# Kernel optimization log

Hardware: AMD Instinct MI355X
Metric: run time of the kernel (lower is better)

Reference implementation:

```python
import math
import jax, jax.numpy as jnp
import numpy as np

N_EMBD = 1024
N_HEAD = 16
HEAD_DIM = N_EMBD // N_HEAD
B, T = 4, 2048
LN_EPS = 1e-5


def setup_inputs() -> dict:
    key = jax.random.key(0)
    ks = jax.random.split(key, 20)
    s = 0.02
    d = {
        'x': jax.random.normal(ks[0], (B, T, N_EMBD), jnp.float32),
        'Wq': jax.random.normal(ks[1], (N_EMBD, N_EMBD), jnp.float32) * s,
        'bq': jnp.zeros((N_EMBD,), jnp.float32),
        'Wk': jax.random.normal(ks[2], (N_EMBD, N_EMBD), jnp.float32) * s,
        'bk': jnp.zeros((N_EMBD,), jnp.float32),
        'Wv': jax.random.normal(ks[3], (N_EMBD, N_EMBD), jnp.float32) * s,
        'bv': jnp.zeros((N_EMBD,), jnp.float32),
        'Wo': jax.random.normal(ks[4], (N_EMBD, N_EMBD), jnp.float32) * s,
        'bo': jnp.zeros((N_EMBD,), jnp.float32),
        'ln1_g': jnp.ones((N_EMBD,), jnp.float32),
        'ln1_b': jnp.zeros((N_EMBD,), jnp.float32),
        'ln2_g': jnp.ones((N_EMBD,), jnp.float32),
        'ln2_b': jnp.zeros((N_EMBD,), jnp.float32),
        'W_fc': jax.random.normal(ks[5], (N_EMBD, 4 * N_EMBD), jnp.float32) * s,
        'b_fc': jnp.zeros((4 * N_EMBD,), jnp.float32),
        'W_proj': jax.random.normal(ks[6], (4 * N_EMBD, N_EMBD), jnp.float32) * s,
        'b_proj': jnp.zeros((N_EMBD,), jnp.float32),
    }
    return d


def _layernorm(x, g, b):
    mu = jnp.mean(x, axis=-1, keepdims=True)
    var = jnp.var(x, axis=-1, keepdims=True)
    return (x - mu) * jax.lax.rsqrt(var + LN_EPS) * g + b


def _new_gelu(x):
    c = math.sqrt(2.0 / math.pi)
    return 0.5 * x * (1.0 + jnp.tanh(c * (x + 0.044715 * x ** 3)))


def _attn(x, Wq, bq, Wk, bk, Wv, bv, Wo, bo):
    Bq, Tq, C = x.shape
    def heads(y):  # (B,T,C) -> (B,H,T,D)
        return y.reshape(Bq, Tq, N_HEAD, HEAD_DIM).transpose(0, 2, 1, 3)
    q = heads(x @ Wq + bq)
    k = heads(x @ Wk + bk)
    v = heads(x @ Wv + bv)
    scores = jnp.einsum('bhqd,bhkd->bhqk', q, k) / math.sqrt(HEAD_DIM)
    causal = jnp.tril(jnp.ones((Tq, Tq), bool))
    scores = jnp.where(causal, scores, -jnp.inf)
    w = jax.nn.softmax(scores, axis=-1)
    av = jnp.einsum('bhqk,bhkd->bhqd', w, v)
    av = av.transpose(0, 2, 1, 3).reshape(Bq, Tq, C)
    return av @ Wo + bo


def reference(x, Wq, bq, Wk, bk, Wv, bv, Wo, bo, ln1_g, ln1_b, ln2_g, ln2_b, W_fc, b_fc, W_proj, b_proj):
    x = x + _attn(_layernorm(x, ln1_g, ln1_b), Wq, bq, Wk, bk, Wv, bv, Wo, bo)
    h = _layernorm(x, ln2_g, ln2_b)
    x = x + (_new_gelu(h @ W_fc + b_fc) @ W_proj + b_proj)
    return x
```

## Files before the change

### kernel.cpp

```cpp
#include <hip/hip_runtime.h>

typedef __attribute__((ext_vector_type(8))) short short8;
typedef __attribute__((ext_vector_type(4))) short short4v;
typedef __attribute__((ext_vector_type(4))) float floatx4;
typedef unsigned short u16;

#define MFMA16(a,b,c) __builtin_amdgcn_mfma_f32_16x16x32_bf16(a,b,c,0,0,0)

typedef const __attribute__((address_space(1))) void* gas1;
typedef __attribute__((address_space(3))) void* las3;
static __device__ __forceinline__ void glds16(const void* g, void* l){
  __builtin_amdgcn_global_load_lds((gas1)g, (las3)l, 16, 0, 0);
}

static __device__ __forceinline__ u16 f2b(float f){
  union { float f; unsigned int u; } c; c.f = f;
  unsigned int u = c.u;
  u += 0x7fffu + ((u >> 16) & 1u);
  return (u16)(u >> 16);
}

__global__ __launch_bounds__(256) void transpose_cvt(
    const float* __restrict__ W, u16* __restrict__ Wt, int K, int N){
  __shared__ float tile[32][33];
  const int tx = threadIdx.x & 31;
  const int ty = threadIdx.x >> 5;
  const int nx = blockIdx.x * 32, kx = blockIdx.y * 32;
  #pragma unroll
  for (int i = ty; i < 32; i += 8)
    tile[i][tx] = W[(size_t)(kx + i) * N + nx + tx];
  __syncthreads();
  #pragma unroll
  for (int i = ty; i < 32; i += 8)
    Wt[(size_t)(nx + i) * K + kx + tx] = f2b(tile[tx][i]);
}

__global__ __launch_bounds__(256) void ln_kernel(
    const float* __restrict__ x, const float* __restrict__ g,
    const float* __restrict__ b, u16* __restrict__ out){
  const int row = blockIdx.x, tid = threadIdx.x;
  const float4 v = reinterpret_cast<const float4*>(x + (size_t)row * 1024)[tid];
  float s  = v.x + v.y + v.z + v.w;
  float s2 = v.x*v.x + v.y*v.y + v.z*v.z + v.w*v.w;
  #pragma unroll
  for (int off = 1; off < 64; off <<= 1){
    s  += __shfl_xor(s,  off);
    s2 += __shfl_xor(s2, off);
  }
  __shared__ float red[8];
  const int wave = tid >> 6, lane = tid & 63;
  if (lane == 0){ red[wave] = s; red[4 + wave] = s2; }
  __syncthreads();
  s  = red[0] + red[1] + red[2] + red[3];
  s2 = red[4] + red[5] + red[6] + red[7];
  const float mu  = s * (1.f/1024.f);
  const float var = s2 * (1.f/1024.f) - mu * mu;
  const float rs  = rsqrtf(var + 1e-5f);
  const float4 gg = reinterpret_cast<const float4*>(g)[tid];
  const float4 bb = reinterpret_cast<const float4*>(b)[tid];
  ushort4 o;
  o.x = f2b((v.x - mu) * rs * gg.x + bb.x);
  o.y = f2b((v.y - mu) * rs * gg.y + bb.y);
  o.z = f2b((v.z - mu) * rs * gg.z + bb.z);
  o.w = f2b((v.w - mu) * rs * gg.w + bb.w);
  reinterpret_cast<ushort4*>(out + (size_t)row * 1024)[tid] = o;
}

__global__ __launch_bounds__(256) void bias_concat(
    const float* __restrict__ bq, const float* __restrict__ bk,
    const float* __restrict__ bv, float* __restrict__ o){
  const int i = blockIdx.x * 256 + threadIdx.x;
  if (i < 1024) o[i] = bq[i];
  else if (i < 2048) o[i] = bk[i - 1024];
  else if (i < 3072) o[i] = bv[i - 2048];
}

template<bool GELU, bool RES, bool OUTBF, bool QKVMODE>
__global__ __launch_bounds__(256) void gemm128(
    const u16* __restrict__ A, const u16* __restrict__ Bt,
    const float* __restrict__ bias, const float* __restrict__ bias2,
    const float* __restrict__ bias3,
    const float* __restrict__ res,
    float* __restrict__ outF, u16* __restrict__ outB,
    u16* __restrict__ vtb,
    int M, int N, int K)
{
  __shared__ __attribute__((aligned(16))) u16 sA[2][128 * 32];
  __shared__ __attribute__((aligned(16))) u16 sB[2][128 * 32];
  const int tid  = threadIdx.x;
  const int wave = tid >> 6, lane = tid & 63, quad = lane >> 4, l16 = lane & 15;
  const int m0 = blockIdx.x * 128, n0 = blockIdx.y * 128;
  const int wm = (wave >> 1) * 64, wn = (wave & 1) * 64;

  const int scol = ((lane & 3) ^ ((lane >> 3) & 3)) * 8;
  const size_t aoff = (size_t)(m0 + wave*32 + (lane >> 2)) * K + scol;
  const size_t boff = (size_t)(n0 + wave*32 + (lane >> 2)) * K + scol;
  const size_t half = (size_t)16 * K;
  u16* alp = sA[0] + wave * 1024;
  u16* blp = sB[0] + wave * 1024;
  const int qx = (quad ^ ((l16 >> 1) & 3)) * 8;

  floatx4 acc[4][4];
  #pragma unroll
  for (int i = 0; i < 4; i++)
    #pragma unroll
    for (int nt = 0; nt < 4; nt++) acc[i][nt] = floatx4{0.f,0.f,0.f,0.f};

  for (int k0 = 0; k0 < K; k0 += 64){
    #pragma unroll
    for (int c = 0; c < 2; c++){
      glds16(A  + aoff + k0 + c*32,        alp + c*4096);
      glds16(A  + aoff + k0 + c*32 + half, alp + c*4096 + 512);
      glds16(Bt + boff + k0 + c*32,        blp + c*4096);
      glds16(Bt + boff + k0 + c*32 + half, blp + c*4096 + 512);
    }
    __syncthreads();
    #pragma unroll
    for (int c = 0; c < 2; c++){
      short8 af[4], bf[4];
      #pragma unroll
      for (int i = 0; i < 4; i++)
        af[i] = *reinterpret_cast<const short8*>(&sA[c][(wm + i*16 + l16)*32 + qx]);
      #pragma unroll
      for (int nt = 0; nt < 4; nt++)
        bf[nt] = *reinterpret_cast<const short8*>(&sB[c][(wn + nt*16 + l16)*32 + qx]);
      #pragma unroll
      for (int i = 0; i < 4; i++)
        #pragma unroll
        for (int nt = 0; nt < 4; nt++)
          acc[i][nt] = MFMA16(af[i], bf[nt], acc[i][nt]);
    }
    __syncthreads();
  }

  if (QKVMODE && n0 >= 2048){
    #pragma unroll
    for (int nt = 0; nt < 4; nt++){
      const int hd = n0 + wn + nt*16 + l16 - 2048;
      const float bi = bias3[hd];
      u16* vcol = vtb + (size_t)(hd >> 6) * 131072 + (size_t)(hd & 63) * 2048;
      #pragma unroll
      for (int i = 0; i < 4; i++){
        const int t0 = m0 + wm + i*16 + quad*4;
        const int bb = t0 >> 11, tt = t0 & 2047;
        short4v pk;
        #pragma unroll
        for (int r = 0; r < 4; r++) pk[r] = (short)f2b(acc[i][nt][r] + bi);
        *reinterpret_cast<short4v*>(vcol + (size_t)bb * 2097152 + tt) = pk;
      }
    }
    return;
  }

  #pragma unroll
  for (int nt = 0; nt < 4; nt++){
    const int col = n0 + wn + nt*16 + l16;
    float bi;
    if (QKVMODE) bi = (col < 1024) ? bias[col] : bias2[col-1024];
    else         bi = bias[col];
    #pragma unroll
    for (int i = 0; i < 4; i++){
      #pragma unroll
      for (int r = 0; r < 4; r++){
        const int row = m0 + wm + i*16 + quad*4 + r;
        float val = acc[i][nt][r] + bi;
        if (GELU){
          const float t = 0.7978845608028654f * (val + 0.044715f * val * val * val);
          val = val / (1.f + __expf(-2.f * t));
        }
        if (RES) val += res[(size_t)row * N + col];
        if (OUTBF) outB[(size_t)row * N + col] = f2b(val);
        else       outF[(size_t)row * N + col] = val;
      }
    }
  }
}

__global__ __launch_bounds__(256) void attn_kernel(
    const u16* __restrict__ qkv, const u16* __restrict__ vtb,
    u16* __restrict__ O)
{
  constexpr int T = 2048, LDQ = 3072, LDP = 72;
  __shared__ __attribute__((aligned(16))) u16 sK0[64*32], sK1[64*32];
  __shared__ __attribute__((aligned(16))) u16 sV0[64*32], sV1[64*32];
  __shared__ __attribute__((aligned(16))) u16 sP[4][16*LDP];

  const int tid = threadIdx.x, wave = tid >> 6, lane = tid & 63;
  const int quad = lane >> 4, l16 = lane & 15;
  const int q0 = (gridDim.x - 1 - blockIdx.x) * 128;
  const int bh = blockIdx.y, b = bh >> 4, h = bh & 15;
  const u16* Qp = qkv + (size_t)b * T * LDQ + h * 64;
  const u16* Kp = Qp + 1024;
  const u16* Vt = vtb + (size_t)bh * 64 * T;

  const int qx = (quad ^ ((l16 >> 1) & 3)) * 8;

  int qg[2]; qg[0] = q0 + wave*16 + l16; qg[1] = qg[0] + 64;
  short8 qf[2][2];
  #pragma unroll
  for (int g = 0; g < 2; g++){
    qf[g][0] = *reinterpret_cast<const short8*>(&Qp[(size_t)qg[g]*LDQ + quad*8]);
    qf[g][1] = *reinterpret_cast<const short8*>(&Qp[(size_t)qg[g]*LDQ + 32 + quad*8]);
  }

  float m_i[2] = {-INFINITY, -INFINITY}, l_i[2] = {0.f, 0.f};
  floatx4 o_acc[2][4];
  #pragma unroll
  for (int g = 0; g < 2; g++)
    #pragma unroll
    for (int nt = 0; nt < 4; nt++) o_acc[g][nt] = floatx4{0.f,0.f,0.f,0.f};

  const int srow = wave*16 + (lane >> 2);
  const int scol = ((lane & 3) ^ ((lane >> 3) & 3)) * 8;
  const int asrc = (lane & 48) | (quad * 4);

  for (int k0 = 0; k0 < q0 + 128; k0 += 64){
    glds16(Kp + (size_t)(k0 + srow)*LDQ + scol,      sK0 + wave*512);
    glds16(Kp + (size_t)(k0 + srow)*LDQ + 32 + scol, sK1 + wave*512);
    glds16(Vt + (size_t)srow*T + k0 + scol,          sV0 + wave*512);
    glds16(Vt + (size_t)srow*T + k0 + 32 + scol,     sV1 + wave*512);
    __syncthreads();

    #pragma unroll
    for (int g = 0; g < 2; g++){
      if (g == 0 && k0 > q0) continue;

      float s[4][4];
      #pragma unroll
      for (int sub = 0; sub < 4; sub++){
        floatx4 sa = floatx4{0.f,0.f,0.f,0.f};
        const short8 kf0 = *reinterpret_cast<const short8*>(&sK0[(sub*16 + l16)*32 + qx]);
        const short8 kf1 = *reinterpret_cast<const short8*>(&sK1[(sub*16 + l16)*32 + qx]);
        sa = MFMA16(kf0, qf[g][0], sa);
        sa = MFMA16(kf1, qf[g][1], sa);
        #pragma unroll
        for (int r = 0; r < 4; r++) s[sub][r] = sa[r];
      }
      if (k0 == q0 + g*64){
        #pragma unroll
        for (int sub = 0; sub < 4; sub++)
          #pragma unroll
          for (int r = 0; r < 4; r++){
            const int kk = k0 + sub*16 + quad*4 + r;
            if (kk > qg[g]) s[sub][r] = -1e30f;
          }
      }

      float mx = s[0][0];
      #pragma unroll
      for (int sub = 0; sub < 4; sub++)
        #pragma unroll
        for (int r = 0; r < 4; r++) mx = fmaxf(mx, s[sub][r]);
      mx = fmaxf(mx, __shfl_xor(mx, 16));
      mx = fmaxf(mx, __shfl_xor(mx, 32));
      const float mnew  = fmaxf(m_i[g], mx);
      const float alpha = __expf(0.125f * (m_i[g] - mnew));
      float p[4][4], rowsum = 0.f;
      #pragma unroll
      for (int sub = 0; sub < 4; sub++)
        #pragma unroll
        for (int r = 0; r < 4; r++){
          p[sub][r] = __expf(0.125f * (s[sub][r] - mnew));
          rowsum += p[sub][r];
        }
      rowsum += __shfl_xor(rowsum, 16);
      rowsum += __shfl_xor(rowsum, 32);
      l_i[g] = l_i[g] * alpha + rowsum;
      m_i[g] = mnew;

      float arow[4];
      #pragma unroll
      for (int r = 0; r < 4; r++) arow[r] = __shfl(alpha, asrc + r);
      #pragma unroll
      for (int nt = 0; nt < 4; nt++)
        #pragma unroll
        for (int r = 0; r < 4; r++) o_acc[g][nt][r] *= arow[r];

      #pragma unroll
      for (int sub = 0; sub < 4; sub++){
        short4v pk;
        pk[0] = (short)f2b(p[sub][0]); pk[1] = (short)f2b(p[sub][1]);
        pk[2] = (short)f2b(p[sub][2]); pk[3] = (short)f2b(p[sub][3]);
        *reinterpret_cast<short4v*>(&sP[wave][l16*LDP + sub*16 + quad*4]) = pk;
      }
      const short8 pf0 = *reinterpret_cast<const short8*>(&sP[wave][l16*LDP + quad*8]);
      const short8 pf1 = *reinterpret_cast<const short8*>(&sP[wave][l16*LDP + 32 + quad*8]);
      #pragma unroll
      for (int nt = 0; nt < 4; nt++){
        const short8 vf0 = *reinterpret_cast<const short8*>(&sV0[(nt*16 + l16)*32 + qx]);
        const short8 vf1 = *reinterpret_cast<const short8*>(&sV1[(nt*16 + l16)*32 + qx]);
        o_acc[g][nt] = MFMA16(pf0, vf0, o_acc[g][nt]);
        o_acc[g][nt] = MFMA16(pf1, vf1, o_acc[g][nt]);
      }
    }
    __syncthreads();
  }

  #pragma unroll
  for (int g = 0; g < 2; g++){
    float lrow[4];
    #pragma unroll
    for (int r = 0; r < 4; r++) lrow[r] = __shfl(l_i[g], asrc + r);
    #pragma unroll
    for (int nt = 0; nt < 4; nt++){
      #pragma unroll
      for (int r = 0; r < 4; r++){
        const int row = q0 + g*64 + wave*16 + quad*4 + r;
        O[(size_t)(b*T + row)*1024 + h*64 + nt*16 + l16] = f2b(o_acc[g][nt][r] / lrow[r]);
      }
    }
  }
}

extern "C" void kernel_launch(void* const* d_in, const int* in_sizes, int n_in,
                              void* d_out, int out_size, void* d_ws, size_t ws_size,
                              hipStream_t stream){
  const float* x      = (const float*)d_in[0];
  const float* Wq     = (const float*)d_in[1];
  const float* bq     = (const float*)d_in[2];
  const float* Wk     = (const float*)d_in[3];
  const float* bk     = (const float*)d_in[4];
  const float* Wv     = (const float*)d_in[5];
  const float* bv     = (const float*)d_in[6];
  const float* Wo     = (const float*)d_in[7];
  const float* bo     = (const float*)d_in[8];
  const float* ln1_g  = (const float*)d_in[9];
  const float* ln1_b  = (const float*)d_in[10];
  const float* ln2_g  = (const float*)d_in[11];
  const float* ln2_b  = (const float*)d_in[12];
  const float* W_fc   = (const float*)d_in[13];
  const float* b_fc   = (const float*)d_in[14];
  const float* W_proj = (const float*)d_in[15];
  const float* b_proj = (const float*)d_in[16];
  float* out = (float*)d_out;
  char* ws = (char*)d_ws;
  const size_t MB = 1024 * 1024;

  u16* bufA  = (u16*)(ws);
  u16* qkvb  = (u16*)(ws + 16*MB);
  u16* vtb   = (u16*)(ws + 64*MB);
  u16* fcb   = (u16*)(ws + 16*MB);
  float* x2  = out;
  u16* Wqkvt = (u16*)(ws + 80*MB);
  u16* Wot   = (u16*)(ws + 86*MB);
  u16* Wfct  = (u16*)(ws + 88*MB);
  u16* Wpjt  = (u16*)(ws + 96*MB);
  float* bqkv= (float*)(ws + 104*MB);

  dim3 tb(256);
  transpose_cvt<<<dim3(32, 32),  tb, 0, stream>>>(Wq,     Wqkvt,             1024, 1024);
  transpose_cvt<<<dim3(32, 32),  tb, 0, stream>>>(Wk,     Wqkvt + 1024*1024, 1024, 1024);
  transpose_cvt<<<dim3(32, 32),  tb, 0, stream>>>(Wv,     Wqkvt + 2048*1024, 1024, 1024);
  transpose_cvt<<<dim3(32, 32),  tb, 0, stream>>>(Wo,     Wot,               1024, 1024);
  transpose_cvt<<<dim3(128, 32), tb, 0, stream>>>(W_fc,   Wfct,              1024, 4096);
  transpose_cvt<<<dim3(32, 128), tb, 0, stream>>>(W_proj, Wpjt,              4096, 1024);
  bias_concat<<<dim3(12), tb, 0, stream>>>(bq, bk, bv, bqkv);

  ln_kernel<<<8192, tb, 0, stream>>>(x, ln1_g, ln1_b, bufA);

  gemm128<false,false,true,true><<<dim3(64,24), tb, 0, stream>>>(
      bufA, Wqkvt, bqkv, bqkv+1024, bqkv+2048, nullptr, nullptr, qkvb, vtb, 8192, 3072, 1024);

  attn_kernel<<<dim3(16, 64), tb, 0, stream>>>(qkvb, vtb, bufA);

  gemm128<false,true,false,false><<<dim3(64,8), tb, 0, stream>>>(
      bufA, Wot, bo, nullptr, nullptr, x, x2, nullptr, nullptr, 8192, 1024, 1024);

  ln_kernel<<<8192, tb, 0, stream>>>(x2, ln2_g, ln2_b, bufA);

  gemm128<true,false,true,false><<<dim3(64,32), tb, 0, stream>>>(
      bufA, Wfct, b_fc, nullptr, nullptr, nullptr, nullptr, fcb, nullptr, 8192, 4096, 1024);

  gemm128<false,true,false,false><<<dim3(64,8), tb, 0, stream>>>(
      fcb, Wpjt, b_proj, nullptr, nullptr, x2, out, nullptr, nullptr, 8192, 1024, 4096);
}
```

Before: 612.7 us.

## Double-buffer K/V tiles in attention and remap blocks for causal load balance

```diff
diff --git a/kernel.cpp b/kernel.cpp
--- a/kernel.cpp
+++ b/kernel.cpp
@@ -181,14 +181,22 @@
     u16* __restrict__ O)
 {
   constexpr int T = 2048, LDQ = 3072, LDP = 72;
-  __shared__ __attribute__((aligned(16))) u16 sK0[64*32], sK1[64*32];
-  __shared__ __attribute__((aligned(16))) u16 sV0[64*32], sV1[64*32];
+  __shared__ __attribute__((aligned(16))) u16 sK[2][2][64*32];
+  __shared__ __attribute__((aligned(16))) u16 sV[2][2][64*32];
   __shared__ __attribute__((aligned(16))) u16 sP[4][16*LDP];
 
   const int tid = threadIdx.x, wave = tid >> 6, lane = tid & 63;
   const int quad = lane >> 4, l16 = lane & 15;
-  const int q0 = (gridDim.x - 1 - blockIdx.x) * 128;
-  const int bh = blockIdx.y, b = bh >> 4, h = bh & 15;
+
+  const int lin = blockIdx.y * 16 + blockIdx.x;
+  const int j = lin & 15;
+  const int bh = lin >> 4;
+  const int kk4 = bh >> 4;
+  const int jj = (j + ((kk4 & 2) << 2)) & 15;
+  const int qt = (kk4 & 1) ? (15 - jj) : jj;
+  const int q0 = qt * 128;
+  const int b = bh >> 4, h = bh & 15;
+
   const u16* Qp = qkv + (size_t)b * T * LDQ + h * 64;
   const u16* Kp = Qp + 1024;
   const u16* Vt = vtb + (size_t)bh * 64 * T;
@@ -214,12 +222,25 @@
   const int scol = ((lane & 3) ^ ((lane >> 3) & 3)) * 8;
   const int asrc = (lane & 48) | (quad * 4);
 
-  for (int k0 = 0; k0 < q0 + 128; k0 += 64){
-    glds16(Kp + (size_t)(k0 + srow)*LDQ + scol,      sK0 + wave*512);
-    glds16(Kp + (size_t)(k0 + srow)*LDQ + 32 + scol, sK1 + wave*512);
-    glds16(Vt + (size_t)srow*T + k0 + scol,          sV0 + wave*512);
-    glds16(Vt + (size_t)srow*T + k0 + 32 + scol,     sV1 + wave*512);
+  const int kend = q0 + 128;
+
+  {
+    glds16(Kp + (size_t)srow*LDQ + scol,      sK[0][0] + wave*512);
+    glds16(Kp + (size_t)srow*LDQ + 32 + scol, sK[0][1] + wave*512);
+    glds16(Vt + (size_t)srow*T + scol,        sV[0][0] + wave*512);
+    glds16(Vt + (size_t)srow*T + 32 + scol,   sV[0][1] + wave*512);
+  }
+
+  int buf = 0;
+  for (int k0 = 0; k0 < kend; k0 += 64, buf ^= 1){
     __syncthreads();
+    if (k0 + 64 < kend){
+      const int kn = k0 + 64;
+      glds16(Kp + (size_t)(kn + srow)*LDQ + scol,      sK[buf^1][0] + wave*512);
+      glds16(Kp + (size_t)(kn + srow)*LDQ + 32 + scol, sK[buf^1][1] + wave*512);
+      glds16(Vt + (size_t)srow*T + kn + scol,          sV[buf^1][0] + wave*512);
+      glds16(Vt + (size_t)srow*T + kn + 32 + scol,     sV[buf^1][1] + wave*512);
+    }
 
     #pragma unroll
     for (int g = 0; g < 2; g++){
@@ -229,8 +250,8 @@
       #pragma unroll
       for (int sub = 0; sub < 4; sub++){
         floatx4 sa = floatx4{0.f,0.f,0.f,0.f};
-        const short8 kf0 = *reinterpret_cast<const short8*>(&sK0[(sub*16 + l16)*32 + qx]);
-        const short8 kf1 = *reinterpret_cast<const short8*>(&sK1[(sub*16 + l16)*32 + qx]);
+        const short8 kf0 = *reinterpret_cast<const short8*>(&sK[buf][0][(sub*16 + l16)*32 + qx]);
+        const short8 kf1 = *reinterpret_cast<const short8*>(&sK[buf][1][(sub*16 + l16)*32 + qx]);
         sa = MFMA16(kf0, qf[g][0], sa);
         sa = MFMA16(kf1, qf[g][1], sa);
         #pragma unroll
@@ -241,8 +262,8 @@
         for (int sub = 0; sub < 4; sub++)
           #pragma unroll
           for (int r = 0; r < 4; r++){
-            const int kk = k0 + sub*16 + quad*4 + r;
-            if (kk > qg[g]) s[sub][r] = -1e30f;
+            const int kidx = k0 + sub*16 + quad*4 + r;
+            if (kidx > qg[g]) s[sub][r] = -1e30f;
           }
       }
 
@@ -287,13 +308,12 @@
       const short8 pf1 = *reinterpret_cast<const short8*>(&sP[wave][l16*LDP + 32 + quad*8]);
       #pragma unroll
       for (int nt = 0; nt < 4; nt++){
-        const short8 vf0 = *reinterpret_cast<const short8*>(&sV0[(nt*16 + l16)*32 + qx]);
-        const short8 vf1 = *reinterpret_cast<const short8*>(&sV1[(nt*16 + l16)*32 + qx]);
+        const short8 vf0 = *reinterpret_cast<const short8*>(&sV[buf][0][(nt*16 + l16)*32 + qx]);
+        const short8 vf1 = *reinterpret_cast<const short8*>(&sV[buf][1][(nt*16 + l16)*32 + qx]);
         o_acc[g][nt] = MFMA16(pf0, vf0, o_acc[g][nt]);
         o_acc[g][nt] = MFMA16(pf1, vf1, o_acc[g][nt]);
       }
     }
-    __syncthreads();
   }
 
   #pragma unroll
```

Result: faster. 559.1 us (-8.8%).
